# Kernel tuning notes

Hardware: AMD Instinct MI355X
Metric: run time of the kernel (lower is better)

The kernel has to match this reference:

```python
import jax, jax.numpy as jnp
import numpy as np

DECAY = 0.99
EPS = 1e-05
N_EMBED = 4096  # codebook_size
DIM = 128       # latent_size
N = 131072      # flattened batch of vectors


def setup_inputs() -> dict:
    key = jax.random.key(0)
    k1, k2, k3, k4 = jax.random.split(key, 4)
    x = jax.random.normal(k1, (N, DIM), dtype=jnp.float32)
    embed = jax.random.normal(k2, (DIM, N_EMBED), dtype=jnp.float32)
    cluster_size = jax.random.uniform(k3, (N_EMBED,), dtype=jnp.float32)
    embed_avg = jax.random.normal(k4, (DIM, N_EMBED), dtype=jnp.float32)
    return {"x": x, "embed": embed, "cluster_size": cluster_size, "embed_avg": embed_avg}


def reference(x, embed, cluster_size, embed_avg):
    dist = (x * x).sum(1, keepdims=True) - 2.0 * (x @ embed) + (embed * embed).sum(0, keepdims=True)
    embed_ind = jnp.argmin(dist, axis=1)  # == (-dist).max(1) index

    # Quantize with the PRE-update codebook (matches torch ordering)
    quantize = jnp.take(embed.T, embed_ind, axis=0)  # [N, DIM]

    # EMA statistics via scatter-reduce (one-hot sum / x^T @ one-hot)
    ones = jnp.ones_like(embed_ind, dtype=x.dtype)
    embed_onehot_sum = jax.ops.segment_sum(ones, embed_ind, num_segments=N_EMBED)        # [K]
    embed_sum = jax.ops.segment_sum(x, embed_ind, num_segments=N_EMBED).T               # [DIM, K]

    cluster_size_new = cluster_size * DECAY + (1.0 - DECAY) * embed_onehot_sum
    embed_avg_new = embed_avg * DECAY + (1.0 - DECAY) * embed_sum

    # low_usage_threshold == -1 -> reinit branch disabled; just count small clusters
    n_small_clusters = (cluster_size_new < 1.0).sum()

    # Laplace-smoothed normalization of the EMA codebook
    n = cluster_size_new.sum()
    cs_norm = (cluster_size_new + EPS) / (n + N_EMBED * EPS) * n
    embed_new = embed_avg_new / cs_norm[None, :]

    quant_loss = jnp.mean((jax.lax.stop_gradient(quantize) - x) ** 2)
    quantize_st = x + jax.lax.stop_gradient(quantize - x)  # straight-through

    return quantize_st, quant_loss, n_small_clusters, embed_ind, embed_new, cluster_size_new, embed_avg_new
```

## Files before the change

kernel.cpp:

```cpp
#include <hip/hip_runtime.h>

constexpr int   NVEC  = 131072;
constexpr int   DIMC  = 128;
constexpr int   KC    = 4096;
constexpr float DECAYC = 0.99f;
constexpr float OMDECAY = 0.01f;
constexpr float EPSC  = 1e-5f;
constexpr float MARGIN1 = 0.4f;
constexpr float MARGIN2 = 0.02f;

typedef __bf16 v8bf __attribute__((ext_vector_type(8)));
typedef float  v4f  __attribute__((ext_vector_type(4)));

__device__ __forceinline__ void async_copy16(const void* gp, void* lds_wave_base, int lane) {
#if __has_builtin(__builtin_amdgcn_global_load_lds)
    __builtin_amdgcn_global_load_lds(
        (const __attribute__((address_space(1))) unsigned int*)gp,
        (__attribute__((address_space(3))) unsigned int*)lds_wave_base, 16, 0, 0);
#else
    ((v8bf*)lds_wave_base)[lane] = *(const v8bf*)gp;
#endif
}

__global__ __launch_bounds__(256) void split_e_kernel(const float* __restrict__ embed,
                                                      __bf16* __restrict__ ehT,
                                                      __bf16* __restrict__ elT,
                                                      float* __restrict__ nhe2) {
    __shared__ __bf16 sh_h[64 * 130];
    __shared__ __bf16 sh_l[64 * 130];
    __shared__ float  sh_n[4][64];
    const int tid = threadIdx.x;
    const int kbase = blockIdx.x * 64;
    const int kloc = tid & 63;
    float nacc = 0.f;
    for (int it = 0; it < 32; ++it) {
        int d = it * 4 + (tid >> 6);
        float v = embed[(size_t)d * KC + kbase + kloc];
        __bf16 h = (__bf16)v;
        __bf16 l = (__bf16)(v - (float)h);
        sh_h[kloc * 130 + d] = h;
        sh_l[kloc * 130 + d] = l;
        nacc = fmaf(v, v, nacc);
    }
    sh_n[tid >> 6][kloc] = nacc;
    __syncthreads();
    if (tid < 64)
        nhe2[kbase + tid] = -0.5f * (sh_n[0][tid] + sh_n[1][tid] + sh_n[2][tid] + sh_n[3][tid]);
    for (int it = 0; it < 32; ++it) {
        int idx = it * 256 + tid;
        int k = idx >> 7;
        int d = idx & 127;
        ehT[(size_t)(kbase + k) * DIMC + d] = sh_h[k * 130 + d];
        elT[(size_t)(kbase + k) * DIMC + d] = sh_l[k * 130 + d];
    }
}

__global__ __launch_bounds__(256, 2) void phase1_kernel(
    const float* __restrict__ x, const __bf16* __restrict__ ehT,
    const float* __restrict__ nhe2,
    float* __restrict__ out_indf, int* __restrict__ ws_ind, float* __restrict__ ws_gap)
{
    __shared__ v8bf E[1024];
    const int tid  = threadIdx.x;
    const int wave = tid >> 6;
    const int lane = tid & 63;
    const int c    = lane & 15;
    const int q    = lane >> 4;
    const int rowBase = blockIdx.x * 128 + wave * 32;

    v8bf ah[2][4];
#pragma unroll
    for (int t = 0; t < 2; ++t)
#pragma unroll
        for (int s = 0; s < 4; ++s) {
            const float* p = x + (size_t)(rowBase + t * 16 + c) * DIMC + s * 32 + q * 8;
            float4 v0 = *reinterpret_cast<const float4*>(p);
            float4 v1 = *reinterpret_cast<const float4*>(p + 4);
            float vv[8] = {v0.x, v0.y, v0.z, v0.w, v1.x, v1.y, v1.z, v1.w};
            v8bf h;
#pragma unroll
            for (int j = 0; j < 8; ++j) h[j] = (__bf16)vv[j];
            ah[t][s] = h;
        }

    const __bf16* ph = ehT + (size_t)(tid & 15) * DIMC + (tid >> 4) * 8;

    float b1[8], b2[8]; int i1[8];
#pragma unroll
    for (int s = 0; s < 8; ++s) { b1[s] = -3.4e38f; b2[s] = -3.4e38f; i1[s] = 0; }

    for (int chunk = 0; chunk < KC / 64; ++chunk) {
        float nhc[4];
#pragma unroll
        for (int t4 = 0; t4 < 4; ++t4) nhc[t4] = nhe2[chunk * 64 + t4 * 16 + c];
#pragma unroll
        for (int it = 0; it < 4; ++it)
            async_copy16(ph + (size_t)it * 16 * DIMC, &E[it * 256 + wave * 64], lane);
        ph += (size_t)64 * DIMC;
        __syncthreads();

#pragma unroll
        for (int ct = 0; ct < 4; ++ct) {
            const float nh = nhc[ct];
            v4f acc0 = {nh, nh, nh, nh};
            v4f acc1 = {nh, nh, nh, nh};
#pragma unroll
            for (int s = 0; s < 4; ++s) {
                v8bf bh = E[ct * 256 + s * 64 + lane];
                acc0 = __builtin_amdgcn_mfma_f32_16x16x32_bf16(ah[0][s], bh, acc0, 0, 0, 0);
                acc1 = __builtin_amdgcn_mfma_f32_16x16x32_bf16(ah[1][s], bh, acc1, 0, 0, 0);
            }
            const int colG = chunk * 64 + ct * 16 + c;
#pragma unroll
            for (int r = 0; r < 4; ++r) {
                float sc = acc0[r];
                float ob = b1[r];
                b2[r] = __builtin_amdgcn_fmed3f(ob, b2[r], sc);
                b1[r] = fmaxf(ob, sc);
                i1[r] = (sc > ob) ? colG : i1[r];
                float sc1 = acc1[r];
                float ob1 = b1[4 + r];
                b2[4 + r] = __builtin_amdgcn_fmed3f(ob1, b2[4 + r], sc1);
                b1[4 + r] = fmaxf(ob1, sc1);
                i1[4 + r] = (sc1 > ob1) ? colG : i1[4 + r];
            }
        }
        __syncthreads();
    }

#pragma unroll
    for (int off = 1; off < 16; off <<= 1) {
#pragma unroll
        for (int s = 0; s < 8; ++s) {
            float ob1 = __shfl_xor(b1[s], off, 64);
            int   oi1 = __shfl_xor(i1[s], off, 64);
            float ob2 = __shfl_xor(b2[s], off, 64);
            if (ob1 > b1[s] || (ob1 == b1[s] && oi1 < i1[s])) {
                b2[s] = fmaxf(b1[s], ob2); b1[s] = ob1; i1[s] = oi1;
            } else {
                b2[s] = fmaxf(b2[s], ob1);
            }
        }
    }
    if (c == 0) {
#pragma unroll
        for (int s = 0; s < 8; ++s) {
            int t = s >> 2, r = s & 3;
            int row = rowBase + t * 16 + q * 4 + r;
            ws_ind[row]   = i1[s];
            out_indf[row] = (float)i1[s];
            ws_gap[row]   = b1[s] - b2[s];
        }
    }
}

__global__ __launch_bounds__(256) void fh_kernel(const float* __restrict__ ws_gap,
                                                 const int* __restrict__ ws_ind,
                                                 int* __restrict__ ws_nflag,
                                                 int* __restrict__ ws_list,
                                                 int* __restrict__ cnt) {
    int n = blockIdx.x * 256 + threadIdx.x;
    if (ws_gap[n] < MARGIN1) {
        int p = atomicAdd(ws_nflag, 1);
        ws_list[p] = n;
    } else {
        atomicAdd(&cnt[ws_ind[n]], 1);
    }
}

__global__ __launch_bounds__(256, 2) void rescore_mfma_kernel(
    const float* __restrict__ x, const __bf16* __restrict__ ehT,
    const __bf16* __restrict__ elT, const float* __restrict__ nhe2,
    const int* __restrict__ ws_list, const int* __restrict__ ws_nflag,
    float* __restrict__ out_indf, int* __restrict__ ws_ind,
    int* __restrict__ ws_nflag2, int* __restrict__ ws_list2, int* __restrict__ cnt)
{
    const int nflag = *ws_nflag;
    if (blockIdx.x * 128 >= nflag) return;

    __shared__ v8bf E[2048];
    const int tid  = threadIdx.x;
    const int wave = tid >> 6;
    const int lane = tid & 63;
    const int c    = lane & 15;
    const int q    = lane >> 4;
    const int gBase = blockIdx.x * 128 + wave * 32;

    v8bf ah[2][4], al[2][4];
#pragma unroll
    for (int t = 0; t < 2; ++t) {
        int gi  = gBase + t * 16 + c;
        int row = ws_list[gi < nflag ? gi : nflag - 1];
#pragma unroll
        for (int s = 0; s < 4; ++s) {
            const float* p = x + (size_t)row * DIMC + s * 32 + q * 8;
            float4 v0 = *reinterpret_cast<const float4*>(p);
            float4 v1 = *reinterpret_cast<const float4*>(p + 4);
            float vv[8] = {v0.x, v0.y, v0.z, v0.w, v1.x, v1.y, v1.z, v1.w};
            v8bf h, l;
#pragma unroll
            for (int j = 0; j < 8; ++j) {
                __bf16 hh = (__bf16)vv[j];
                h[j] = hh;
                l[j] = (__bf16)(vv[j] - (float)hh);
            }
            ah[t][s] = h; al[t][s] = l;
        }
    }

    const __bf16* ph = ehT + (size_t)(tid & 15) * DIMC + (tid >> 4) * 8;
    const __bf16* pl = elT + (size_t)(tid & 15) * DIMC + (tid >> 4) * 8;

    float b1[8], b2[8]; int i1[8];
#pragma unroll
    for (int s = 0; s < 8; ++s) { b1[s] = -3.4e38f; b2[s] = -3.4e38f; i1[s] = 0; }

    for (int chunk = 0; chunk < KC / 64; ++chunk) {
        float nhc[4];
#pragma unroll
        for (int t4 = 0; t4 < 4; ++t4) nhc[t4] = nhe2[chunk * 64 + t4 * 16 + c];
#pragma unroll
        for (int it = 0; it < 4; ++it) {
            async_copy16(ph + (size_t)it * 16 * DIMC, &E[it * 256 + wave * 64], lane);
            async_copy16(pl + (size_t)it * 16 * DIMC, &E[1024 + it * 256 + wave * 64], lane);
        }
        ph += (size_t)64 * DIMC;
        pl += (size_t)64 * DIMC;
        __syncthreads();

#pragma unroll
        for (int ct = 0; ct < 4; ++ct) {
            const float nh = nhc[ct];
            v4f acc0 = {nh, nh, nh, nh};
            v4f acc1 = {nh, nh, nh, nh};
#pragma unroll
            for (int s = 0; s < 4; ++s) {
                v8bf bh = E[ct * 256 + s * 64 + lane];
                v8bf bl = E[1024 + ct * 256 + s * 64 + lane];
                acc0 = __builtin_amdgcn_mfma_f32_16x16x32_bf16(ah[0][s], bh, acc0, 0, 0, 0);
                acc1 = __builtin_amdgcn_mfma_f32_16x16x32_bf16(ah[1][s], bh, acc1, 0, 0, 0);
                acc0 = __builtin_amdgcn_mfma_f32_16x16x32_bf16(al[0][s], bh, acc0, 0, 0, 0);
                acc1 = __builtin_amdgcn_mfma_f32_16x16x32_bf16(al[1][s], bh, acc1, 0, 0, 0);
                acc0 = __builtin_amdgcn_mfma_f32_16x16x32_bf16(ah[0][s], bl, acc0, 0, 0, 0);
                acc1 = __builtin_amdgcn_mfma_f32_16x16x32_bf16(ah[1][s], bl, acc1, 0, 0, 0);
            }
            const int colG = chunk * 64 + ct * 16 + c;
#pragma unroll
            for (int r = 0; r < 4; ++r) {
                float sc = acc0[r];
                float ob = b1[r];
                b2[r] = __builtin_amdgcn_fmed3f(ob, b2[r], sc);
                b1[r] = fmaxf(ob, sc);
                i1[r] = (sc > ob) ? colG : i1[r];
                float sc1 = acc1[r];
                float ob1 = b1[4 + r];
                b2[4 + r] = __builtin_amdgcn_fmed3f(ob1, b2[4 + r], sc1);
                b1[4 + r] = fmaxf(ob1, sc1);
                i1[4 + r] = (sc1 > ob1) ? colG : i1[4 + r];
            }
        }
        __syncthreads();
    }

#pragma unroll
    for (int off = 1; off < 16; off <<= 1) {
#pragma unroll
        for (int s = 0; s < 8; ++s) {
            float ob1 = __shfl_xor(b1[s], off, 64);
            int   oi1 = __shfl_xor(i1[s], off, 64);
            float ob2 = __shfl_xor(b2[s], off, 64);
            if (ob1 > b1[s] || (ob1 == b1[s] && oi1 < i1[s])) {
                b2[s] = fmaxf(b1[s], ob2); b1[s] = ob1; i1[s] = oi1;
            } else {
                b2[s] = fmaxf(b2[s], ob1);
            }
        }
    }
    if (c == 0) {
#pragma unroll
        for (int s = 0; s < 8; ++s) {
            int t = s >> 2, r = s & 3;
            int gi = gBase + t * 16 + q * 4 + r;
            if (gi < nflag) {
                int row = ws_list[gi];
                ws_ind[row]   = i1[s];
                out_indf[row] = (float)i1[s];
                if (b1[s] - b2[s] < MARGIN2) {
                    int p = atomicAdd(ws_nflag2, 1);
                    ws_list2[p] = row;
                } else {
                    atomicAdd(&cnt[i1[s]], 1);
                }
            }
        }
    }
}

__global__ __launch_bounds__(256) void rescore_exact_kernel(
    const float* __restrict__ x, const float* __restrict__ embed,
    const float* __restrict__ nhe2, const int* __restrict__ ws_list,
    const int* __restrict__ ws_nflag, int* __restrict__ ws_ind,
    float* __restrict__ out_indf, int* __restrict__ cnt)
{
    __shared__ float xs[16][128];
    __shared__ float redv[4][16];
    __shared__ int   redi[4][16];
    const int tid  = threadIdx.x;
    const int lane = tid & 63;
    const int wave = tid >> 6;
    const int nflag = *ws_nflag;

    for (int g = blockIdx.x; g * 16 < nflag; g += gridDim.x) {
        const int base = g * 16;
        const int cntg = min(16, nflag - base);
        __syncthreads();
#pragma unroll
        for (int it = 0; it < 2; ++it) {
            int idx = it * 256 + tid;
            int r   = idx >> 5;
            int d4  = (idx & 31) * 4;
            int row = ws_list[base + (r < cntg ? r : 0)];
            float4 v = *reinterpret_cast<const float4*>(x + (size_t)row * DIMC + d4);
            *reinterpret_cast<float4*>(&xs[r][d4]) = v;
        }
        __syncthreads();

        float b1[16]; int i1[16];
#pragma unroll
        for (int r = 0; r < 16; ++r) { b1[r] = -3.4e38f; i1[r] = 0; }

#pragma unroll 1
        for (int iter = 0; iter < 4; ++iter) {
            const int col4 = iter * 1024 + tid * 4;
            float4 acc[16];
#pragma unroll
            for (int r = 0; r < 16; ++r) acc[r] = make_float4(0.f, 0.f, 0.f, 0.f);
#pragma unroll 4
            for (int d = 0; d < DIMC; ++d) {
                float4 ev = *reinterpret_cast<const float4*>(embed + (size_t)d * KC + col4);
#pragma unroll
                for (int r = 0; r < 16; ++r) {
                    float xv = xs[r][d];
                    acc[r].x = fmaf(ev.x, xv, acc[r].x);
                    acc[r].y = fmaf(ev.y, xv, acc[r].y);
                    acc[r].z = fmaf(ev.z, xv, acc[r].z);
                    acc[r].w = fmaf(ev.w, xv, acc[r].w);
                }
            }
            float4 nh = *reinterpret_cast<const float4*>(nhe2 + col4);
#pragma unroll
            for (int r = 0; r < 16; ++r) {
                float s0 = acc[r].x + nh.x;
                float s1 = acc[r].y + nh.y;
                float s2 = acc[r].z + nh.z;
                float s3 = acc[r].w + nh.w;
                if (s0 > b1[r]) { b1[r] = s0; i1[r] = col4 + 0; }
                if (s1 > b1[r]) { b1[r] = s1; i1[r] = col4 + 1; }
                if (s2 > b1[r]) { b1[r] = s2; i1[r] = col4 + 2; }
                if (s3 > b1[r]) { b1[r] = s3; i1[r] = col4 + 3; }
            }
        }
#pragma unroll
        for (int off = 1; off < 64; off <<= 1)
#pragma unroll
            for (int r = 0; r < 16; ++r) {
                float ob = __shfl_xor(b1[r], off, 64);
                int   oi = __shfl_xor(i1[r], off, 64);
                if (ob > b1[r] || (ob == b1[r] && oi < i1[r])) { b1[r] = ob; i1[r] = oi; }
            }
        if (lane == 0)
#pragma unroll
            for (int r = 0; r < 16; ++r) { redv[wave][r] = b1[r]; redi[wave][r] = i1[r]; }
        __syncthreads();
        if (tid < cntg) {
            float bv = redv[0][tid]; int bi = redi[0][tid];
#pragma unroll
            for (int w = 1; w < 4; ++w) {
                float ov = redv[w][tid]; int oi = redi[w][tid];
                if (ov > bv || (ov == bv && oi < bi)) { bv = ov; bi = oi; }
            }
            int row = ws_list[base + tid];
            ws_ind[row]   = bi;
            out_indf[row] = (float)bi;
            atomicAdd(&cnt[bi], 1);
        }
    }
}

__global__ __launch_bounds__(1024) void scan_kernel(const int* __restrict__ cnt,
                                                    int* __restrict__ start,
                                                    int* __restrict__ cursor) {
    __shared__ int sh[1024];
    const int t = threadIdx.x;
    int4 c = *reinterpret_cast<const int4*>(cnt + t * 4);
    int s = c.x + c.y + c.z + c.w;
    sh[t] = s;
    __syncthreads();
    for (int off = 1; off < 1024; off <<= 1) {
        int v = (t >= off) ? sh[t - off] : 0;
        __syncthreads();
        sh[t] += v;
        __syncthreads();
    }
    int s0 = (t == 0) ? 0 : sh[t - 1];
    start[t * 4 + 0] = s0; cursor[t * 4 + 0] = s0; s0 += c.x;
    start[t * 4 + 1] = s0; cursor[t * 4 + 1] = s0; s0 += c.y;
    start[t * 4 + 2] = s0; cursor[t * 4 + 2] = s0; s0 += c.z;
    start[t * 4 + 3] = s0; cursor[t * 4 + 3] = s0;
}

__global__ __launch_bounds__(256) void bucket_kernel(const int* __restrict__ ind,
                                                     int* __restrict__ cursor,
                                                     int* __restrict__ sorted) {
    int n = blockIdx.x * 256 + threadIdx.x;
    int p = atomicAdd(&cursor[ind[n]], 1);
    sorted[p] = n;
}

__global__ __launch_bounds__(1024) void cluster_sum_kernel(
    const float* __restrict__ x, const float* __restrict__ embed,
    const int* __restrict__ sorted, const int* __restrict__ start,
    const int* __restrict__ cnt, float* __restrict__ quant_out,
    float* __restrict__ ws_sum, float* __restrict__ ws_lpart)
{
    const int k   = blockIdx.x;
    const int tid = threadIdx.x;
    const int d   = tid & 127;
    const int grp = tid >> 7;
    const int s0  = start[k];
    const int c   = cnt[k];
    const float e = embed[(size_t)d * KC + k];
    __shared__ int   rows[256];
    __shared__ float partial[8][128];
    __shared__ float lred[16];

    float asum = 0.f;
    float loss = 0.f;

    for (int base = 0; base < c; base += 256) {
        int m = min(256, c - base);
        __syncthreads();
        if (tid < m) rows[tid] = sorted[s0 + base + tid];
        __syncthreads();
        int lo = grp * 32;
        int hi = min(lo + 32, m);
        int i = lo;
        for (; i + 4 <= hi; i += 4) {
            int r0 = rows[i + 0], r1 = rows[i + 1], r2 = rows[i + 2], r3 = rows[i + 3];
            float x0 = x[(size_t)r0 * DIMC + d];
            float x1 = x[(size_t)r1 * DIMC + d];
            float x2 = x[(size_t)r2 * DIMC + d];
            float x3 = x[(size_t)r3 * DIMC + d];
            float d0 = e - x0, d1 = e - x1, d2 = e - x2, d3 = e - x3;
            asum += x0; asum += x1; asum += x2; asum += x3;
            loss = fmaf(d0, d0, loss); loss = fmaf(d1, d1, loss);
            loss = fmaf(d2, d2, loss); loss = fmaf(d3, d3, loss);
            quant_out[(size_t)r0 * DIMC + d] = x0 + d0;
            quant_out[(size_t)r1 * DIMC + d] = x1 + d1;
            quant_out[(size_t)r2 * DIMC + d] = x2 + d2;
            quant_out[(size_t)r3 * DIMC + d] = x3 + d3;
        }
        for (; i < hi; ++i) {
            int r0 = rows[i];
            float x0 = x[(size_t)r0 * DIMC + d];
            float d0 = e - x0;
            asum += x0;
            loss = fmaf(d0, d0, loss);
            quant_out[(size_t)r0 * DIMC + d] = x0 + d0;
        }
    }

    partial[grp][d] = asum;
#pragma unroll
    for (int off = 32; off >= 1; off >>= 1) loss += __shfl_down(loss, off, 64);
    if ((tid & 63) == 0) lred[tid >> 6] = loss;
    __syncthreads();
    if (tid < 128) {
        float s = partial[0][tid];
#pragma unroll
        for (int g2 = 1; g2 < 8; ++g2) s += partial[g2][tid];
        ws_sum[(size_t)tid * KC + k] = s;
    }
    if (tid == 0) {
        float L = 0.f;
#pragma unroll
        for (int w = 0; w < 16; ++w) L += lred[w];
        ws_lpart[k] = L;
    }
}

__global__ __launch_bounds__(1024) void finalize_kernel(
    const float* __restrict__ cs, const int* __restrict__ cnt,
    const float* __restrict__ ws_lpart,
    float* __restrict__ out_loss, float* __restrict__ out_nsmall,
    float* __restrict__ out_csn, float* __restrict__ ws_inv)
{
    const int tid = threadIdx.x;
    float csn_loc[4];
    float lsum = 0.f, lsmall = 0.f, lloss = 0.f;
#pragma unroll
    for (int i = 0; i < 4; ++i) {
        int k = tid + i * 1024;
        float csn = cs[k] * DECAYC + OMDECAY * (float)cnt[k];
        out_csn[k] = csn;
        csn_loc[i] = csn;
        lsum += csn;
        lsmall += (csn < 1.f) ? 1.f : 0.f;
        lloss += ws_lpart[k];
    }
#pragma unroll
    for (int off = 32; off >= 1; off >>= 1) {
        lsum   += __shfl_down(lsum, off, 64);
        lsmall += __shfl_down(lsmall, off, 64);
        lloss  += __shfl_down(lloss, off, 64);
    }
    __shared__ float sh1[16], sh2[16], sh3[16];
    __shared__ float ntot_s;
    if ((tid & 63) == 0) { sh1[tid >> 6] = lsum; sh2[tid >> 6] = lsmall; sh3[tid >> 6] = lloss; }
    __syncthreads();
    if (tid == 0) {
        float tot = 0.f, sm = 0.f, lo = 0.f;
        for (int w = 0; w < 16; ++w) { tot += sh1[w]; sm += sh2[w]; lo += sh3[w]; }
        ntot_s = tot;
        out_nsmall[0] = sm;
        out_loss[0] = lo * (1.0f / ((float)NVEC * (float)DIMC));
    }
    __syncthreads();
    float ntot = ntot_s;
    float scale = (ntot + (float)KC * EPSC) / ntot;
#pragma unroll
    for (int i = 0; i < 4; ++i) {
        int k = tid + i * 1024;
        ws_inv[k] = scale / (csn_loc[i] + EPSC);
    }
}

__global__ __launch_bounds__(256) void ema_embed_kernel(
    const float* __restrict__ ea, const float* __restrict__ ws_sum,
    const float* __restrict__ ws_inv, float* __restrict__ out_embed_new,
    float* __restrict__ out_ean)
{
    size_t i4 = ((size_t)blockIdx.x * 256 + threadIdx.x) * 4;
    float4 a = *reinterpret_cast<const float4*>(ea + i4);
    float4 s = *reinterpret_cast<const float4*>(ws_sum + i4);
    int k = (int)(i4 & (KC - 1));
    float4 inv = *reinterpret_cast<const float4*>(ws_inv + k);
    float e0 = a.x * DECAYC + OMDECAY * s.x;
    float e1 = a.y * DECAYC + OMDECAY * s.y;
    float e2 = a.z * DECAYC + OMDECAY * s.z;
    float e3 = a.w * DECAYC + OMDECAY * s.w;
    *reinterpret_cast<float2*>(out_ean + i4)     = make_float2(e0, e1);
    *reinterpret_cast<float2*>(out_ean + i4 + 2) = make_float2(e2, e3);
    *reinterpret_cast<float2*>(out_embed_new + i4)     = make_float2(e0 * inv.x, e1 * inv.y);
    *reinterpret_cast<float2*>(out_embed_new + i4 + 2) = make_float2(e2 * inv.z, e3 * inv.w);
}

extern "C" void kernel_launch(void* const* d_in, const int* in_sizes, int n_in,
                              void* d_out, int out_size, void* d_ws, size_t ws_size,
                              hipStream_t stream) {
    const float* x     = (const float*)d_in[0];
    const float* embed = (const float*)d_in[1];
    const float* cs    = (const float*)d_in[2];
    const float* ea    = (const float*)d_in[3];

    float* out  = (float*)d_out;
    float* out0 = out;
    float* out1 = out + 16777216;
    float* out2 = out + 16777217;
    float* out3 = out + 16777218;
    float* out4 = out + 16908290;
    float* out5 = out + 17432578;
    float* out6 = out + 17436674;

    float* ws       = (float*)d_ws;
    float* ws_sum   = ws;
    int*   ws_nflag = (int*)(ws + 528385);
    float* ws_inv   = ws + 528388;
    float* nhe2     = ws + 532484;
    int*   ws_cnt_i  = (int*)(ws + 540676);
    int*   ws_nflag2 = (int*)(ws + 544772);
    int*   ws_list2  = (int*)(ws + 548868);
    int*   ws_ind   = (int*)(ws + 1060868);
    float* ws_gap   = ws + 1191940;
    int*   ws_list  = (int*)(ws + 1323012);
    __bf16* ehT     = (__bf16*)(ws + 1454084);
    __bf16* elT     = (__bf16*)(ws + 1716228);
    int*   ws_sorted = (int*)(ws + 1454084);
    int*   ws_start  = (int*)(ws + 1720324);
    int*   ws_cursor = (int*)(ws + 1724420);
    float* ws_lpart  = ws + 1728516;

    hipMemsetAsync(ws_nflag, 0, sizeof(int), stream);
    hipMemsetAsync(ws_nflag2, 0, sizeof(int), stream);
    hipMemsetAsync(ws_cnt_i, 0, KC * sizeof(int), stream);

    hipLaunchKernelGGL(split_e_kernel,   dim3(KC / 64), dim3(256), 0, stream,
                       embed, ehT, elT, nhe2);
    hipLaunchKernelGGL(phase1_kernel,    dim3(NVEC / 128), dim3(256), 0, stream,
                       x, ehT, nhe2, out3, ws_ind, ws_gap);

    hipLaunchKernelGGL(fh_kernel,        dim3(NVEC / 256), dim3(256), 0, stream,
                       ws_gap, ws_ind, ws_nflag, ws_list, ws_cnt_i);
    hipLaunchKernelGGL(rescore_mfma_kernel, dim3(NVEC / 128), dim3(256), 0, stream,
                       x, ehT, elT, nhe2, ws_list, ws_nflag,
                       out3, ws_ind, ws_nflag2, ws_list2, ws_cnt_i);
    hipLaunchKernelGGL(rescore_exact_kernel, dim3(512), dim3(256), 0, stream,
                       x, embed, nhe2, ws_list2, ws_nflag2, ws_ind, out3, ws_cnt_i);

    hipLaunchKernelGGL(scan_kernel,   dim3(1), dim3(1024), 0, stream, ws_cnt_i, ws_start, ws_cursor);
    hipLaunchKernelGGL(bucket_kernel, dim3(NVEC / 256), dim3(256), 0, stream,
                       ws_ind, ws_cursor, ws_sorted);
    hipLaunchKernelGGL(cluster_sum_kernel, dim3(KC), dim3(1024), 0, stream,
                       x, embed, ws_sorted, ws_start, ws_cnt_i, out0, ws_sum, ws_lpart);

    hipLaunchKernelGGL(finalize_kernel, dim3(1), dim3(1024), 0, stream,
                       cs, ws_cnt_i, ws_lpart, out1, out2, out5, ws_inv);
    hipLaunchKernelGGL(ema_embed_kernel, dim3((DIMC * KC) / 1024), dim3(256), 0, stream,
                       ea, ws_sum, ws_inv, out4, out6);
}
```

Baseline: 686.4 us.

## Split cluster sums across four blocks per code, fold memsets into split kernel

Cluster_sum now launches four blocks per codebook entry, each handling a quarter of that cluster's rows, and accumulates into ws_sum and ws_lpart with atomics. The aim is better load balance over uneven cluster sizes. Zeroing of the accumulators and flags moves into split_e_kernel, replacing three hipMemsetAsync calls. Phase1 also doubles its LDS chunk to 128 codes per sync, halving barriers at the cost of more shared memory, and float atomics make the summation order nondeterministic.

```diff
diff --git a/kernel.cpp b/kernel.cpp
--- a/kernel.cpp
+++ b/kernel.cpp
@@ -25,11 +25,24 @@
 __global__ __launch_bounds__(256) void split_e_kernel(const float* __restrict__ embed,
                                                       __bf16* __restrict__ ehT,
                                                       __bf16* __restrict__ elT,
-                                                      float* __restrict__ nhe2) {
+                                                      float* __restrict__ nhe2,
+                                                      float* __restrict__ ws_sum,
+                                                      float* __restrict__ ws_lpart,
+                                                      int* __restrict__ ws_cnt,
+                                                      int* __restrict__ ws_nflag,
+                                                      int* __restrict__ ws_nflag2) {
     __shared__ __bf16 sh_h[64 * 130];
     __shared__ __bf16 sh_l[64 * 130];
     __shared__ float  sh_n[4][64];
     const int tid = threadIdx.x;
+    const int gid = blockIdx.x * 256 + tid;
+#pragma unroll
+    for (int i = 0; i < 8; ++i)
+        *reinterpret_cast<float4*>(ws_sum + (size_t)(gid + i * 16384) * 4) =
+            make_float4(0.f, 0.f, 0.f, 0.f);
+    if (gid < KC) { ws_lpart[gid] = 0.f; ws_cnt[gid] = 0; }
+    if (gid == 0) { *ws_nflag = 0; *ws_nflag2 = 0; }
+
     const int kbase = blockIdx.x * 64;
     const int kloc = tid & 63;
     float nacc = 0.f;
@@ -60,7 +73,7 @@
     const float* __restrict__ nhe2,
     float* __restrict__ out_indf, int* __restrict__ ws_ind, float* __restrict__ ws_gap)
 {
-    __shared__ v8bf E[1024];
+    __shared__ v8bf E[2048];
     const int tid  = threadIdx.x;
     const int wave = tid >> 6;
     const int lane = tid & 63;
@@ -89,18 +102,18 @@
 #pragma unroll
     for (int s = 0; s < 8; ++s) { b1[s] = -3.4e38f; b2[s] = -3.4e38f; i1[s] = 0; }
 
-    for (int chunk = 0; chunk < KC / 64; ++chunk) {
-        float nhc[4];
-#pragma unroll
-        for (int t4 = 0; t4 < 4; ++t4) nhc[t4] = nhe2[chunk * 64 + t4 * 16 + c];
-#pragma unroll
-        for (int it = 0; it < 4; ++it)
+    for (int chunk = 0; chunk < KC / 128; ++chunk) {
+        float nhc[8];
+#pragma unroll
+        for (int t4 = 0; t4 < 8; ++t4) nhc[t4] = nhe2[chunk * 128 + t4 * 16 + c];
+#pragma unroll
+        for (int it = 0; it < 8; ++it)
             async_copy16(ph + (size_t)it * 16 * DIMC, &E[it * 256 + wave * 64], lane);
-        ph += (size_t)64 * DIMC;
-        __syncthreads();
-
-#pragma unroll
-        for (int ct = 0; ct < 4; ++ct) {
+        ph += (size_t)128 * DIMC;
+        __syncthreads();
+
+#pragma unroll
+        for (int ct = 0; ct < 8; ++ct) {
             const float nh = nhc[ct];
             v4f acc0 = {nh, nh, nh, nh};
             v4f acc1 = {nh, nh, nh, nh};
@@ -110,7 +123,7 @@
                 acc0 = __builtin_amdgcn_mfma_f32_16x16x32_bf16(ah[0][s], bh, acc0, 0, 0, 0);
                 acc1 = __builtin_amdgcn_mfma_f32_16x16x32_bf16(ah[1][s], bh, acc1, 0, 0, 0);
             }
-            const int colG = chunk * 64 + ct * 16 + c;
+            const int colG = chunk * 128 + ct * 16 + c;
 #pragma unroll
             for (int r = 0; r < 4; ++r) {
                 float sc = acc0[r];
@@ -423,12 +436,18 @@
     const int* __restrict__ cnt, float* __restrict__ quant_out,
     float* __restrict__ ws_sum, float* __restrict__ ws_lpart)
 {
-    const int k   = blockIdx.x;
+    const int k   = blockIdx.x >> 2;
+    const int seg = blockIdx.x & 3;
     const int tid = threadIdx.x;
     const int d   = tid & 127;
     const int grp = tid >> 7;
-    const int s0  = start[k];
     const int c   = cnt[k];
+    const int Q   = (c + 3) >> 2;
+    const int lo0 = seg * Q;
+    const int hi0 = min(c, lo0 + Q);
+    if (lo0 >= hi0) return;
+    const int s0  = start[k] + lo0;
+    const int len = hi0 - lo0;
     const float e = embed[(size_t)d * KC + k];
     __shared__ int   rows[256];
     __shared__ float partial[8][128];
@@ -437,15 +456,15 @@
     float asum = 0.f;
     float loss = 0.f;
 
-    for (int base = 0; base < c; base += 256) {
-        int m = min(256, c - base);
+    for (int base = 0; base < len; base += 256) {
+        int m = min(256, len - base);
         __syncthreads();
         if (tid < m) rows[tid] = sorted[s0 + base + tid];
         __syncthreads();
-        int lo = grp * 32;
-        int hi = min(lo + 32, m);
-        int i = lo;
-        for (; i + 4 <= hi; i += 4) {
+        int glo = grp * 32;
+        int ghi = min(glo + 32, m);
+        int i = glo;
+        for (; i + 4 <= ghi; i += 4) {
             int r0 = rows[i + 0], r1 = rows[i + 1], r2 = rows[i + 2], r3 = rows[i + 3];
             float x0 = x[(size_t)r0 * DIMC + d];
             float x1 = x[(size_t)r1 * DIMC + d];
@@ -460,7 +479,7 @@
             quant_out[(size_t)r2 * DIMC + d] = x2 + d2;
             quant_out[(size_t)r3 * DIMC + d] = x3 + d3;
         }
-        for (; i < hi; ++i) {
+        for (; i < ghi; ++i) {
             int r0 = rows[i];
             float x0 = x[(size_t)r0 * DIMC + d];
             float d0 = e - x0;
@@ -479,13 +498,13 @@
         float s = partial[0][tid];
 #pragma unroll
         for (int g2 = 1; g2 < 8; ++g2) s += partial[g2][tid];
-        ws_sum[(size_t)tid * KC + k] = s;
+        atomicAdd(&ws_sum[(size_t)tid * KC + k], s);
     }
     if (tid == 0) {
         float L = 0.f;
 #pragma unroll
         for (int w = 0; w < 16; ++w) L += lred[w];
-        ws_lpart[k] = L;
+        atomicAdd(&ws_lpart[k], L);
     }
 }
 
@@ -580,6 +599,7 @@
     int*   ws_cnt_i  = (int*)(ws + 540676);
     int*   ws_nflag2 = (int*)(ws + 544772);
     int*   ws_list2  = (int*)(ws + 548868);
+    float* ws_lpart  = ws + 684036;
     int*   ws_ind   = (int*)(ws + 1060868);
     float* ws_gap   = ws + 1191940;
     int*   ws_list  = (int*)(ws + 1323012);
@@ -588,14 +608,10 @@
     int*   ws_sorted = (int*)(ws + 1454084);
     int*   ws_start  = (int*)(ws + 1720324);
     int*   ws_cursor = (int*)(ws + 1724420);
-    float* ws_lpart  = ws + 1728516;
-
-    hipMemsetAsync(ws_nflag, 0, sizeof(int), stream);
-    hipMemsetAsync(ws_nflag2, 0, sizeof(int), stream);
-    hipMemsetAsync(ws_cnt_i, 0, KC * sizeof(int), stream);
 
     hipLaunchKernelGGL(split_e_kernel,   dim3(KC / 64), dim3(256), 0, stream,
-                       embed, ehT, elT, nhe2);
+                       embed, ehT, elT, nhe2, ws_sum, ws_lpart, ws_cnt_i,
+                       ws_nflag, ws_nflag2);
     hipLaunchKernelGGL(phase1_kernel,    dim3(NVEC / 128), dim3(256), 0, stream,
                        x, ehT, nhe2, out3, ws_ind, ws_gap);
 
@@ -610,7 +626,7 @@
     hipLaunchKernelGGL(scan_kernel,   dim3(1), dim3(1024), 0, stream, ws_cnt_i, ws_start, ws_cursor);
     hipLaunchKernelGGL(bucket_kernel, dim3(NVEC / 256), dim3(256), 0, stream,
                        ws_ind, ws_cursor, ws_sorted);
-    hipLaunchKernelGGL(cluster_sum_kernel, dim3(KC), dim3(1024), 0, stream,
+    hipLaunchKernelGGL(cluster_sum_kernel, dim3(KC * 4), dim3(1024), 0, stream,
                        x, embed, ws_sorted, ws_start, ws_cnt_i, out0, ws_sum, ws_lpart);
 
     hipLaunchKernelGGL(finalize_kernel, dim3(1), dim3(1024), 0, stream,
```

Measured after the change: 753.4 us. 9.8% more time.
